# Optimization experiments

Hardware: AMD Instinct MI355X
Metric: run time of the kernel (lower is better)

The kernel has to match this reference:

```python
import jax, jax.numpy as jnp
import numpy as np
from jax import lax

TAU = 2.0      # LIF membrane time constant
VTH = 0.5      # spike threshold
ALPHA = 4.0    # sigmoid surrogate gradient sharpness (spikingjelly default)
EPS = 1e-5     # BatchNorm eps
HEADS = 8

@jax.custom_vjp
def _spike(x):
    return (x >= 0.0).astype(x.dtype)

def _spike_fwd(x):
    return _spike(x), x

def _spike_bwd(x, g):
    s = jax.nn.sigmoid(ALPHA * x)
    return (g * ALPHA * s * (1.0 - s),)

_spike.defvjp(_spike_fwd, _spike_bwd)

def lif(x_seq):
    # multi-step LIF, decay_input=True, hard reset to 0, detach_reset=True
    def step(v, x):
        v = v + (x - v) / TAU
        s = _spike(v - VTH)
        v = v * (1.0 - lax.stop_gradient(s))
        return v, s
    _, s_seq = lax.scan(step, jnp.zeros_like(x_seq[0]), x_seq)
    return s_seq

def bn(x, gamma, beta, mean, var):
    # inference-mode BatchNorm over channel axis 2 of [T,B,C,H,W]
    sh = (1, 1, -1, 1, 1)
    scale = gamma.reshape(sh) / jnp.sqrt(var.reshape(sh) + EPS)
    return (x - mean.reshape(sh)) * scale + beta.reshape(sh)

def conv1x1(x, w, b=None):
    y = jnp.einsum('oc,tbchw->tbohw', w, x)
    if b is not None:
        y = y + b.reshape(1, 1, -1, 1, 1)
    return y

def setup_inputs() -> dict:
    key = jax.random.key(0)
    T, B, C, H, W = 4, 8, 384, 32, 32
    ks = jax.random.split(key, 20)
    s = 1.0 / np.sqrt(C)
    d = {
        'x': jax.random.normal(ks[0], (T, B, C, H, W), jnp.float32),
        'q_w': jax.random.normal(ks[1], (C, C), jnp.float32) * s,
        'k_w': jax.random.normal(ks[2], (C, C), jnp.float32) * s,
        'v_w': jax.random.normal(ks[3], (C, C), jnp.float32) * s,
        'th_w': jax.random.normal(ks[4], (HEADS, HEADS), jnp.float32) * (1.0 / np.sqrt(HEADS)),
        'proj_w': jax.random.normal(ks[5], (C, C), jnp.float32) * s,
        'proj_b': jax.random.normal(ks[6], (C,), jnp.float32) * 0.01,
    }
    for i, p in enumerate(['q', 'k', 'v', 'proj']):
        kk = jax.random.split(ks[7 + i], 4)
        d[f'{p}_gamma'] = 1.0 + 0.1 * jax.random.normal(kk[0], (C,), jnp.float32)
        d[f'{p}_beta'] = 0.1 * jax.random.normal(kk[1], (C,), jnp.float32)
        d[f'{p}_mean'] = 0.1 * jax.random.normal(kk[2], (C,), jnp.float32)
        d[f'{p}_var'] = jax.random.uniform(kk[3], (C,), jnp.float32, 0.5, 1.5)
    return d

def reference(x, q_w, k_w, v_w, th_w, proj_w, proj_b,
              q_gamma, q_beta, q_mean, q_var,
              k_gamma, k_beta, k_mean, k_var,
              v_gamma, v_beta, v_mean, v_var,
              proj_gamma, proj_beta, proj_mean, proj_var):
    T, B, C, H, W = x.shape
    hd = C // HEADS
    N = H * W
    identity = x
    xs = lif(x)  # shortcut_lif

    def branch(w, g, be, m, va):
        return lif(bn(conv1x1(xs, w), g, be, m, va))

    def split_heads(t):  # [T,B,C,H,W] -> [T,B,heads,N,hd]
        return t.reshape(T, B, HEADS, hd, N).transpose(0, 1, 2, 4, 3)

    q = split_heads(branch(q_w, q_gamma, q_beta, q_mean, q_var))
    k = split_heads(branch(k_w, k_gamma, k_beta, k_mean, k_var))
    v = split_heads(branch(v_w, v_gamma, v_beta, v_mean, v_var))

    kv = (k * v).sum(axis=3)                      # [T,B,heads,hd]
    kv = jnp.einsum('oh,tbhd->tbod', th_w, kv)     # talking heads (Conv1d 1x1, no bias)
    kv = lif(kv)[:, :, :, None, :]                 # [T,B,heads,1,hd]

    x_att = q * kv                                 # broadcast over N
    x_att = x_att.transpose(0, 1, 2, 4, 3).reshape(T, B, C, H, W)
    out = bn(conv1x1(x_att, proj_w, proj_b), proj_gamma, proj_beta, proj_mean, proj_var)
    return out + identity
```

## Files before the change

### kernel.cpp

```cpp
#include <hip/hip_runtime.h>
#include <stdint.h>


typedef unsigned short u16;
typedef __attribute__((ext_vector_type(8))) short short8v;
typedef __attribute__((ext_vector_type(4))) float f32x4;

#define AS1 __attribute__((address_space(1)))
#define AS3 __attribute__((address_space(3)))

__device__ __forceinline__ void async16(const void* g, void* l) {
    __builtin_amdgcn_global_load_lds((const AS1 unsigned int*)g,
                                     (AS3 unsigned int*)l, 16, 0, 0);
}
__device__ __forceinline__ f32x4 mfma_bf16(short8v a, short8v b, f32x4 c) {
    return __builtin_amdgcn_mfma_f32_16x16x32_bf16(a, b, c, 0, 0, 0);
}
__device__ __forceinline__ f32x4 mfma_f16(short8v a, short8v b, f32x4 c) {
    return __builtin_amdgcn_mfma_f32_16x16x32_f16(a, b, c, 0, 0, 0);
}

__device__ __forceinline__ u16 f2bf(float f) {
    uint32_t x = __float_as_uint(f);
    return (u16)((x + 0x7FFFu + ((x >> 16) & 1u)) >> 16);
}

#define SPIKE_H ((u16)0x3C00)
#define SPIKE_B ((u16)0x3F80)

__global__ void prep_kernel(const float* __restrict__ qw, const float* __restrict__ kw,
                            const float* __restrict__ vw, const float* __restrict__ pw,
                            u16* __restrict__ Ah, u16* __restrict__ Aproj) {
    int id = blockIdx.x * 256 + threadIdx.x;
    if (id >= 1152 * 384) return;
    int m = id / 384, c = id % 384;
    int br = m / 384, o = m % 384;
    const float* W = (br == 0) ? qw : (br == 1) ? kw : vw;
    float w = W[o * 384 + c];
    union H { _Float16 h; u16 u; } u0, u1;
    u0.h = (_Float16)w;
    float r1 = w - (float)u0.h;
    u1.h = (_Float16)r1;
    u16* row = Ah + (size_t)m * 768;
    row[c] = u0.u;
    row[384 + c] = u1.u;
    if (br == 0) Aproj[o * 384 + c] = f2bf(pw[o * 384 + c]);
}

__global__ __launch_bounds__(256) void lifx_kernel(const float* __restrict__ x,
                                                   u16* __restrict__ xs) {
    __shared__ u16 Tr[64 * 72];
    int b = blockIdx.z, c0 = blockIdx.y * 64, n0 = blockIdx.x * 64;
    int tid = threadIdx.x;
    int nj = (tid & 15) * 4;
    int ci = tid >> 4;
    float v[4][4];
#pragma unroll
    for (int p = 0; p < 4; p++)
#pragma unroll
        for (int e = 0; e < 4; e++) v[p][e] = 0.0f;

    for (int t = 0; t < 4; t++) {
#pragma unroll
        for (int p = 0; p < 4; p++) {
            const float* src = x + ((size_t)((t * 8 + b) * 384 + c0 + p * 16 + ci)) * 1024 + n0 + nj;
            float4 xv = *(const float4*)src;
            float xa[4] = {xv.x, xv.y, xv.z, xv.w};
#pragma unroll
            for (int e = 0; e < 4; e++) {
                float vv = v[p][e];
                vv = __fadd_rn(vv, __fmul_rn(__fsub_rn(xa[e], vv), 0.5f));
                bool sp = (vv >= 0.5f);
                v[p][e] = sp ? 0.0f : vv;
                Tr[(nj + e) * 72 + p * 16 + ci] = sp ? SPIKE_H : (u16)0;
            }
        }
        __syncthreads();
#pragma unroll
        for (int p = 0; p < 4; p++) {
            int nr = p * 16 + (tid >> 4);
            int c4 = (tid & 15) * 4;
            *(ushort4*)(xs + ((size_t)((t * 8 + b) * 1024 + n0 + nr)) * 384 + c0 + c4) =
                *(const ushort4*)&Tr[nr * 72 + c4];
        }
        __syncthreads();
    }
}

__global__ __launch_bounds__(256, 2) void qkv_kernel(
    const u16* __restrict__ Ah, const u16* __restrict__ xs,
    u16* __restrict__ qs, u16* __restrict__ ks, u16* __restrict__ vs,
    const float* __restrict__ qg, const float* __restrict__ qb, const float* __restrict__ qm, const float* __restrict__ qv,
    const float* __restrict__ kg, const float* __restrict__ kb, const float* __restrict__ km, const float* __restrict__ kvr,
    const float* __restrict__ vg, const float* __restrict__ vb, const float* __restrict__ vm, const float* __restrict__ vvr) {
    __shared__ __align__(16) u16 At[2][8192];
    __shared__ __align__(16) u16 Bt[2][8192];
    __shared__ __align__(16) float bnS[128];
    __shared__ __align__(16) float bnM[128];
    __shared__ __align__(16) float bnB[128];

    int b = blockIdx.z, mt = blockIdx.y, nt = blockIdx.x;
    int m0 = mt * 128, n0 = nt * 128;
    int branch = mt / 3, o0 = (mt % 3) * 128;
    int tid = threadIdx.x, wave = tid >> 6, lane = tid & 63;
    int l15 = lane & 15, quad = lane >> 4;
    int wm = (wave & 1) * 64, wn = (wave >> 1) * 64;

    const float* g_ = (branch == 0) ? qg : (branch == 1) ? kg : vg;
    const float* be_ = (branch == 0) ? qb : (branch == 1) ? kb : vb;
    const float* m_ = (branch == 0) ? qm : (branch == 1) ? km : vm;
    const float* v_ = (branch == 0) ? qv : (branch == 1) ? kvr : vvr;
    u16* dstp = (branch == 0) ? qs : (branch == 1) ? ks : vs;

    if (tid < 128) {
        int o = o0 + tid;
        bnS[tid] = g_[o] / sqrtf(v_[o] + 1e-5f);
        bnM[tid] = m_[o];
        bnB[tid] = be_[o];
    }

    auto stage = [&](int s) {
        int st = s / 12, kkb = s % 12;
        int buf = s & 1;
        int kk = kkb * 64;
        int ck = (kk >= 384) ? kk - 384 : kk;
        const u16* Bsrc = xs + ((size_t)((st * 8 + b) * 1024 + n0)) * 384;
#pragma unroll
        for (int ii = 0; ii < 4; ii++) {
            int l = ii * 256 + tid;
            int row = l >> 3;
            int cs = (l & 7) ^ (row & 7);
            async16(Ah + (size_t)(m0 + row) * 768 + kk + cs * 8, &At[buf][l * 8]);
            async16(Bsrc + (size_t)row * 384 + ck + cs * 8, &Bt[buf][l * 8]);
        }
    };

    float vmem[4][4][4];
#pragma unroll
    for (int i = 0; i < 4; i++)
#pragma unroll
        for (int j = 0; j < 4; j++)
#pragma unroll
            for (int e = 0; e < 4; e++) vmem[i][j][e] = 0.0f;

    stage(0);
    __syncthreads();

    for (int t = 0; t < 4; t++) {
        f32x4 acc[4][4];
#pragma unroll
        for (int i = 0; i < 4; i++)
#pragma unroll
            for (int j = 0; j < 4; j++) acc[i][j] = (f32x4){0.f, 0.f, 0.f, 0.f};

        for (int kkb = 0; kkb < 12; kkb++) {
            int s = t * 12 + kkb;
            int buf = s & 1;
            if (s + 1 < 48) stage(s + 1);
#pragma unroll
            for (int h = 0; h < 2; h++) {
                short8v af[4], bfr[4];
#pragma unroll
                for (int i = 0; i < 4; i++) {
                    int row = wm + i * 16 + l15;
                    int ch = (h * 4 + quad) ^ (row & 7);
                    af[i] = *(const short8v*)&At[buf][row * 64 + ch * 8];
                }
#pragma unroll
                for (int j = 0; j < 4; j++) {
                    int nr = wn + j * 16 + l15;
                    int ch = (h * 4 + quad) ^ (nr & 7);
                    bfr[j] = *(const short8v*)&Bt[buf][nr * 64 + ch * 8];
                }
#pragma unroll
                for (int i = 0; i < 4; i++)
#pragma unroll
                    for (int j = 0; j < 4; j++) acc[i][j] = mfma_f16(af[i], bfr[j], acc[i][j]);
            }
            __syncthreads();
        }

        size_t rb = (size_t)((t * 8 + b) * 1024 + n0);
#pragma unroll
        for (int i = 0; i < 4; i++) {
            int co = wm + i * 16 + quad * 4;
            float4 sc4 = *(const float4*)&bnS[co];
            float4 mn4 = *(const float4*)&bnM[co];
            float4 bt4 = *(const float4*)&bnB[co];
            float scA[4] = {sc4.x, sc4.y, sc4.z, sc4.w};
            float mnA[4] = {mn4.x, mn4.y, mn4.z, mn4.w};
            float btA[4] = {bt4.x, bt4.y, bt4.z, bt4.w};
#pragma unroll
            for (int j = 0; j < 4; j++) {
                int n = wn + j * 16 + l15;
                u16 sv[4];
#pragma unroll
                for (int e = 0; e < 4; e++) {
                    float a = acc[i][j][e];
                    a = __fadd_rn(__fmul_rn(__fsub_rn(a, mnA[e]), scA[e]), btA[e]);
                    float vv = vmem[i][j][e];
                    vv = __fadd_rn(vv, __fmul_rn(__fsub_rn(a, vv), 0.5f));
                    bool sp = (vv >= 0.5f);
                    vmem[i][j][e] = sp ? 0.0f : vv;
                    sv[e] = sp ? SPIKE_B : (u16)0;
                }
                ushort4 s4;
                s4.x = sv[0]; s4.y = sv[1]; s4.z = sv[2]; s4.w = sv[3];
                *(ushort4*)(dstp + (rb + n) * 384 + o0 + co) = s4;
            }
        }
    }
}

__global__ void kvred_kernel(const u16* __restrict__ ks, const u16* __restrict__ vs,
                             float* __restrict__ r) {
    __shared__ float red[384];
    int tb = blockIdx.y, nc = blockIdx.x;
    int tid = threadIdx.x;
    int rr = tid / 48, c8 = tid % 48;
    red[tid] = 0.0f;
    __syncthreads();

    float cnt[8];
#pragma unroll
    for (int e = 0; e < 8; e++) cnt[e] = 0.0f;

    size_t base = ((size_t)(tb * 1024 + nc * 64 + rr)) * 384 + c8 * 8;
#pragma unroll 2
    for (int it = 0; it < 8; it++) {
        size_t off = base + (size_t)it * 8 * 384;
        uint4 ka = *(const uint4*)(ks + off);
        uint4 va = *(const uint4*)(vs + off);
        uint32_t w0 = ka.x & va.x, w1 = ka.y & va.y, w2 = ka.z & va.z, w3 = ka.w & va.w;
        const uint32_t S = SPIKE_B;
        if ((w0 & 0xFFFFu) == S) cnt[0] += 1.0f;
        if ((w0 >> 16) == S)     cnt[1] += 1.0f;
        if ((w1 & 0xFFFFu) == S) cnt[2] += 1.0f;
        if ((w1 >> 16) == S)     cnt[3] += 1.0f;
        if ((w2 & 0xFFFFu) == S) cnt[4] += 1.0f;
        if ((w2 >> 16) == S)     cnt[5] += 1.0f;
        if ((w3 & 0xFFFFu) == S) cnt[6] += 1.0f;
        if ((w3 >> 16) == S)     cnt[7] += 1.0f;
    }
#pragma unroll
    for (int e = 0; e < 8; e++) atomicAdd(&red[c8 * 8 + e], cnt[e]);
    __syncthreads();
    atomicAdd(&r[tb * 384 + tid], red[tid]);
}

__global__ void talking_kernel(const float* __restrict__ r, const float* __restrict__ th,
                               u16* __restrict__ kvs) {
    int id = blockIdx.x * 256 + threadIdx.x;
    if (id >= 8 * 384) return;
    int b = id / 384, c = id % 384;
    int oh = c / 48, d = c % 48;
    float v = 0.0f;
    for (int t = 0; t < 4; t++) {
        const float* rr = r + (t * 8 + b) * 384 + d;
        float s = 0.0f;
#pragma unroll
        for (int h = 0; h < 8; h++) s = __fmaf_rn(th[oh * 8 + h], rr[h * 48], s);
        v = __fadd_rn(v, __fmul_rn(__fsub_rn(s, v), 0.5f));
        bool sp = (v >= 0.5f);
        v = sp ? 0.0f : v;
        kvs[(t * 8 + b) * 384 + c] = sp ? SPIKE_B : (u16)0;
    }
}

__global__ __launch_bounds__(256, 2) void proj_kernel(
    const u16* __restrict__ Aproj, const u16* __restrict__ qs, const u16* __restrict__ kvs,
    const float* __restrict__ xin,
    const float* __restrict__ pb, const float* __restrict__ pg, const float* __restrict__ pbe,
    const float* __restrict__ pm, const float* __restrict__ pv, float* __restrict__ out) {
    __shared__ __align__(16) u16 At[2][8192];
    __shared__ __align__(16) u16 Bt[2][8192];

    int tb = blockIdx.z, mt = blockIdx.y, nt = blockIdx.x;
    int m0 = mt * 128, n0 = nt * 128;
    int tid = threadIdx.x, wave = tid >> 6, lane = tid & 63;
    int l15 = lane & 15, quad = lane >> 4;
    int wm = (wave & 1) * 64, wn = (wave >> 1) * 64;

    const u16* Bsrc = qs + ((size_t)(tb * 1024 + n0)) * 384;
    const u16* mbase = kvs + tb * 384;

    auto stage = [&](int s) {
        int kk = s * 64;
        int buf = s & 1;
#pragma unroll
        for (int ii = 0; ii < 4; ii++) {
            int l = ii * 256 + tid;
            int row = l >> 3;
            int cs = (l & 7) ^ (row & 7);
            async16(Aproj + (size_t)(m0 + row) * 384 + kk + cs * 8, &At[buf][l * 8]);
            async16(Bsrc + (size_t)row * 384 + kk + cs * 8, &Bt[buf][l * 8]);
        }
    };

    f32x4 acc[4][4];
#pragma unroll
    for (int i = 0; i < 4; i++)
#pragma unroll
        for (int j = 0; j < 4; j++) acc[i][j] = (f32x4){0.f, 0.f, 0.f, 0.f};

    stage(0);
    __syncthreads();

    for (int kkb = 0; kkb < 6; kkb++) {
        int buf = kkb & 1;
        int kk = kkb * 64;
        if (kkb + 1 < 6) stage(kkb + 1);
#pragma unroll
        for (int h = 0; h < 2; h++) {
            int g = h * 4 + quad;
            short8v msk = *(const short8v*)(mbase + kk + g * 8);
            short8v af[4], bfr[4];
#pragma unroll
            for (int i = 0; i < 4; i++) {
                int row = wm + i * 16 + l15;
                int ch = g ^ (row & 7);
                af[i] = *(const short8v*)&At[buf][row * 64 + ch * 8];
            }
#pragma unroll
            for (int j = 0; j < 4; j++) {
                int nr = wn + j * 16 + l15;
                int ch = g ^ (nr & 7);
                bfr[j] = *(const short8v*)&Bt[buf][nr * 64 + ch * 8] & msk;
            }
#pragma unroll
            for (int i = 0; i < 4; i++)
#pragma unroll
                for (int j = 0; j < 4; j++) acc[i][j] = mfma_bf16(af[i], bfr[j], acc[i][j]);
        }
        __syncthreads();
    }

#pragma unroll
    for (int i = 0; i < 4; i++) {
#pragma unroll
        for (int e = 0; e < 4; e++) {
            int o = m0 + wm + i * 16 + quad * 4 + e;
            float scale = pg[o] / sqrtf(pv[o] + 1e-5f);
            float mean = pm[o], beta = pbe[o], bias = pb[o];
#pragma unroll
            for (int j = 0; j < 4; j++) {
                int n = n0 + wn + j * 16 + l15;
                size_t idx = ((size_t)tb * 384 + o) * 1024 + n;
                float y = __fadd_rn(acc[i][j][e], bias);
                y = __fadd_rn(__fmul_rn(__fsub_rn(y, mean), scale), beta);
                out[idx] = __fadd_rn(y, xin[idx]);
            }
        }
    }
}

extern "C" void kernel_launch(void* const* d_in, const int* in_sizes, int n_in,
                              void* d_out, int out_size, void* d_ws, size_t ws_size,
                              hipStream_t stream) {
    (void)in_sizes; (void)n_in; (void)out_size; (void)ws_size;
    const float* x  = (const float*)d_in[0];
    const float* qw = (const float*)d_in[1];
    const float* kw = (const float*)d_in[2];
    const float* vw = (const float*)d_in[3];
    const float* th = (const float*)d_in[4];
    const float* pw = (const float*)d_in[5];
    const float* pb = (const float*)d_in[6];
    const float* qg = (const float*)d_in[7],  *qbe = (const float*)d_in[8];
    const float* qm = (const float*)d_in[9],  *qv  = (const float*)d_in[10];
    const float* kg = (const float*)d_in[11], *kbe = (const float*)d_in[12];
    const float* km = (const float*)d_in[13], *kv_ = (const float*)d_in[14];
    const float* vg = (const float*)d_in[15], *vbe = (const float*)d_in[16];
    const float* vm = (const float*)d_in[17], *vv_ = (const float*)d_in[18];
    const float* pg = (const float*)d_in[19], *pbe = (const float*)d_in[20];
    const float* pm = (const float*)d_in[21], *pv  = (const float*)d_in[22];
    float* out = (float*)d_out;

    char* w = (char*)d_ws;
    const size_t SPIKES = (size_t)32 * 1024 * 384 * 2;
    u16* xs    = (u16*)(w);
    u16* qs    = (u16*)(w + SPIKES);
    u16* ks    = (u16*)(w + 2 * SPIKES);
    u16* vs    = (u16*)(w + 3 * SPIKES);
    u16* Ah    = (u16*)(w + 4 * SPIKES);
    u16* Aproj = (u16*)(w + 4 * SPIKES + 1769472);
    float* r   = (float*)(w + 4 * SPIKES + 1769472 + 294912);
    u16* kvs   = (u16*)(w + 4 * SPIKES + 1769472 + 294912 + 49152);

    hipMemsetAsync(r, 0, 32 * 384 * sizeof(float), stream);

    prep_kernel<<<1728, 256, 0, stream>>>(qw, kw, vw, pw, Ah, Aproj);
    lifx_kernel<<<dim3(16, 6, 8), 256, 0, stream>>>(x, xs);
    qkv_kernel<<<dim3(8, 9, 8), 256, 0, stream>>>(Ah, xs, qs, ks, vs,
                                                  qg, qbe, qm, qv,
                                                  kg, kbe, km, kv_,
                                                  vg, vbe, vm, vv_);
    kvred_kernel<<<dim3(16, 32), 384, 0, stream>>>(ks, vs, r);
    talking_kernel<<<12, 256, 0, stream>>>(r, th, kvs);
    proj_kernel<<<dim3(8, 3, 32), 256, 0, stream>>>(Aproj, qs, kvs, x, pb, pg, pbe, pm, pv, out);
}
```

Before: 294.5 us.

## Replace LDS-staged GEMM tiles with direct global-to-register fragment loads

```diff
diff --git a/kernel.cpp b/kernel.cpp
--- a/kernel.cpp
+++ b/kernel.cpp
@@ -6,13 +6,6 @@
 typedef __attribute__((ext_vector_type(8))) short short8v;
 typedef __attribute__((ext_vector_type(4))) float f32x4;
 
-#define AS1 __attribute__((address_space(1)))
-#define AS3 __attribute__((address_space(3)))
-
-__device__ __forceinline__ void async16(const void* g, void* l) {
-    __builtin_amdgcn_global_load_lds((const AS1 unsigned int*)g,
-                                     (AS3 unsigned int*)l, 16, 0, 0);
-}
 __device__ __forceinline__ f32x4 mfma_bf16(short8v a, short8v b, f32x4 c) {
     return __builtin_amdgcn_mfma_f32_16x16x32_bf16(a, b, c, 0, 0, 0);
 }
@@ -87,24 +80,18 @@
     }
 }
 
-__global__ __launch_bounds__(256, 2) void qkv_kernel(
+__global__ __launch_bounds__(256) void qkv_kernel(
     const u16* __restrict__ Ah, const u16* __restrict__ xs,
     u16* __restrict__ qs, u16* __restrict__ ks, u16* __restrict__ vs,
     const float* __restrict__ qg, const float* __restrict__ qb, const float* __restrict__ qm, const float* __restrict__ qv,
     const float* __restrict__ kg, const float* __restrict__ kb, const float* __restrict__ km, const float* __restrict__ kvr,
     const float* __restrict__ vg, const float* __restrict__ vb, const float* __restrict__ vm, const float* __restrict__ vvr) {
-    __shared__ __align__(16) u16 At[2][8192];
-    __shared__ __align__(16) u16 Bt[2][8192];
-    __shared__ __align__(16) float bnS[128];
-    __shared__ __align__(16) float bnM[128];
-    __shared__ __align__(16) float bnB[128];
-
-    int b = blockIdx.z, mt = blockIdx.y, nt = blockIdx.x;
-    int m0 = mt * 128, n0 = nt * 128;
-    int branch = mt / 3, o0 = (mt % 3) * 128;
+    int b = blockIdx.z, mt = blockIdx.y;
     int tid = threadIdx.x, wave = tid >> 6, lane = tid & 63;
     int l15 = lane & 15, quad = lane >> 4;
-    int wm = (wave & 1) * 64, wn = (wave >> 1) * 64;
+    int m0 = mt * 64;
+    int branch = mt / 6, o0 = (mt % 6) * 64;
+    int n0 = blockIdx.x * 256 + wave * 64;
 
     const float* g_ = (branch == 0) ? qg : (branch == 1) ? kg : vg;
     const float* be_ = (branch == 0) ? qb : (branch == 1) ? kb : vb;
@@ -112,28 +99,7 @@
     const float* v_ = (branch == 0) ? qv : (branch == 1) ? kvr : vvr;
     u16* dstp = (branch == 0) ? qs : (branch == 1) ? ks : vs;
 
-    if (tid < 128) {
-        int o = o0 + tid;
-        bnS[tid] = g_[o] / sqrtf(v_[o] + 1e-5f);
-        bnM[tid] = m_[o];
-        bnB[tid] = be_[o];
-    }
-
-    auto stage = [&](int s) {
-        int st = s / 12, kkb = s % 12;
-        int buf = s & 1;
-        int kk = kkb * 64;
-        int ck = (kk >= 384) ? kk - 384 : kk;
-        const u16* Bsrc = xs + ((size_t)((st * 8 + b) * 1024 + n0)) * 384;
-#pragma unroll
-        for (int ii = 0; ii < 4; ii++) {
-            int l = ii * 256 + tid;
-            int row = l >> 3;
-            int cs = (l & 7) ^ (row & 7);
-            async16(Ah + (size_t)(m0 + row) * 768 + kk + cs * 8, &At[buf][l * 8]);
-            async16(Bsrc + (size_t)row * 384 + ck + cs * 8, &Bt[buf][l * 8]);
-        }
-    };
+    const u16* Abase = Ah + (size_t)(m0 + l15) * 768 + quad * 8;
 
     float vmem[4][4][4];
 #pragma unroll
@@ -143,56 +109,64 @@
 #pragma unroll
             for (int e = 0; e < 4; e++) vmem[i][j][e] = 0.0f;
 
-    stage(0);
-    __syncthreads();
-
     for (int t = 0; t < 4; t++) {
+        const u16* Bbase = xs + ((size_t)((t * 8 + b) * 1024 + n0 + l15)) * 384 + quad * 8;
+
         f32x4 acc[4][4];
 #pragma unroll
         for (int i = 0; i < 4; i++)
 #pragma unroll
             for (int j = 0; j < 4; j++) acc[i][j] = (f32x4){0.f, 0.f, 0.f, 0.f};
 
-        for (int kkb = 0; kkb < 12; kkb++) {
-            int s = t * 12 + kkb;
-            int buf = s & 1;
-            if (s + 1 < 48) stage(s + 1);
-#pragma unroll
-            for (int h = 0; h < 2; h++) {
-                short8v af[4], bfr[4];
-#pragma unroll
-                for (int i = 0; i < 4; i++) {
-                    int row = wm + i * 16 + l15;
-                    int ch = (h * 4 + quad) ^ (row & 7);
-                    af[i] = *(const short8v*)&At[buf][row * 64 + ch * 8];
-                }
-#pragma unroll
-                for (int j = 0; j < 4; j++) {
-                    int nr = wn + j * 16 + l15;
-                    int ch = (h * 4 + quad) ^ (nr & 7);
-                    bfr[j] = *(const short8v*)&Bt[buf][nr * 64 + ch * 8];
-                }
-#pragma unroll
-                for (int i = 0; i < 4; i++)
-#pragma unroll
-                    for (int j = 0; j < 4; j++) acc[i][j] = mfma_f16(af[i], bfr[j], acc[i][j]);
-            }
-            __syncthreads();
-        }
+        short8v Af[3][4], Bf[3][4];
+
+#define LOADF(HS, SLOT)                                                               \
+        {                                                                             \
+            const int kA = (HS) * 32;                                                 \
+            const int cB = ((HS) % 12) * 32;                                          \
+            _Pragma("unroll")                                                         \
+            for (int i = 0; i < 4; i++)                                               \
+                Af[SLOT][i] = *(const short8v*)(Abase + (size_t)i * (16 * 768) + kA); \
+            _Pragma("unroll")                                                         \
+            for (int j = 0; j < 4; j++)                                               \
+                Bf[SLOT][j] = *(const short8v*)(Bbase + (size_t)j * (16 * 384) + cB); \
+        }
+
+        LOADF(0, 0)
+        LOADF(1, 1)
+        LOADF(2, 2)
+
+#pragma unroll
+        for (int hs = 0; hs < 24; hs++) {
+            const int slot = hs % 3;
+#pragma unroll
+            for (int i = 0; i < 4; i++)
+#pragma unroll
+                for (int j = 0; j < 4; j++)
+                    acc[i][j] = mfma_f16(Af[slot][i], Bf[slot][j], acc[i][j]);
+            if (hs < 21) LOADF(hs + 3, slot)
+        }
+#undef LOADF
 
         size_t rb = (size_t)((t * 8 + b) * 1024 + n0);
 #pragma unroll
         for (int i = 0; i < 4; i++) {
-            int co = wm + i * 16 + quad * 4;
-            float4 sc4 = *(const float4*)&bnS[co];
-            float4 mn4 = *(const float4*)&bnM[co];
-            float4 bt4 = *(const float4*)&bnB[co];
-            float scA[4] = {sc4.x, sc4.y, sc4.z, sc4.w};
-            float mnA[4] = {mn4.x, mn4.y, mn4.z, mn4.w};
-            float btA[4] = {bt4.x, bt4.y, bt4.z, bt4.w};
+            int co = i * 16 + quad * 4;
+            int o = o0 + co;
+            float4 g4 = *(const float4*)(g_ + o);
+            float4 v4 = *(const float4*)(v_ + o);
+            float4 m4 = *(const float4*)(m_ + o);
+            float4 b4 = *(const float4*)(be_ + o);
+            float scA[4], mnA[4], btA[4];
+            scA[0] = g4.x / sqrtf(v4.x + 1e-5f);
+            scA[1] = g4.y / sqrtf(v4.y + 1e-5f);
+            scA[2] = g4.z / sqrtf(v4.z + 1e-5f);
+            scA[3] = g4.w / sqrtf(v4.w + 1e-5f);
+            mnA[0] = m4.x; mnA[1] = m4.y; mnA[2] = m4.z; mnA[3] = m4.w;
+            btA[0] = b4.x; btA[1] = b4.y; btA[2] = b4.z; btA[3] = b4.w;
 #pragma unroll
             for (int j = 0; j < 4; j++) {
-                int n = wn + j * 16 + l15;
+                int n = j * 16 + l15;
                 u16 sv[4];
 #pragma unroll
                 for (int e = 0; e < 4; e++) {
@@ -206,7 +180,7 @@
                 }
                 ushort4 s4;
                 s4.x = sv[0]; s4.y = sv[1]; s4.z = sv[2]; s4.w = sv[3];
-                *(ushort4*)(dstp + (rb + n) * 384 + o0 + co) = s4;
+                *(ushort4*)(dstp + (rb + n) * 384 + o) = s4;
             }
         }
     }
@@ -267,35 +241,20 @@
     }
 }
 
-__global__ __launch_bounds__(256, 2) void proj_kernel(
+__global__ __launch_bounds__(256) void proj_kernel(
     const u16* __restrict__ Aproj, const u16* __restrict__ qs, const u16* __restrict__ kvs,
     const float* __restrict__ xin,
     const float* __restrict__ pb, const float* __restrict__ pg, const float* __restrict__ pbe,
     const float* __restrict__ pm, const float* __restrict__ pv, float* __restrict__ out) {
-    __shared__ __align__(16) u16 At[2][8192];
-    __shared__ __align__(16) u16 Bt[2][8192];
-
-    int tb = blockIdx.z, mt = blockIdx.y, nt = blockIdx.x;
-    int m0 = mt * 128, n0 = nt * 128;
+    int tb = blockIdx.z, mt = blockIdx.y;
     int tid = threadIdx.x, wave = tid >> 6, lane = tid & 63;
     int l15 = lane & 15, quad = lane >> 4;
-    int wm = (wave & 1) * 64, wn = (wave >> 1) * 64;
-
-    const u16* Bsrc = qs + ((size_t)(tb * 1024 + n0)) * 384;
-    const u16* mbase = kvs + tb * 384;
-
-    auto stage = [&](int s) {
-        int kk = s * 64;
-        int buf = s & 1;
-#pragma unroll
-        for (int ii = 0; ii < 4; ii++) {
-            int l = ii * 256 + tid;
-            int row = l >> 3;
-            int cs = (l & 7) ^ (row & 7);
-            async16(Aproj + (size_t)(m0 + row) * 384 + kk + cs * 8, &At[buf][l * 8]);
-            async16(Bsrc + (size_t)row * 384 + kk + cs * 8, &Bt[buf][l * 8]);
-        }
-    };
+    int m0 = mt * 64;
+    int n0 = blockIdx.x * 256 + wave * 64;
+
+    const u16* Abase = Aproj + (size_t)(m0 + l15) * 384 + quad * 8;
+    const u16* Bbase = qs + ((size_t)(tb * 1024 + n0 + l15)) * 384 + quad * 8;
+    const u16* mbase = kvs + tb * 384 + quad * 8;
 
     f32x4 acc[4][4];
 #pragma unroll
@@ -303,48 +262,49 @@
 #pragma unroll
         for (int j = 0; j < 4; j++) acc[i][j] = (f32x4){0.f, 0.f, 0.f, 0.f};
 
-    stage(0);
-    __syncthreads();
-
-    for (int kkb = 0; kkb < 6; kkb++) {
-        int buf = kkb & 1;
-        int kk = kkb * 64;
-        if (kkb + 1 < 6) stage(kkb + 1);
-#pragma unroll
-        for (int h = 0; h < 2; h++) {
-            int g = h * 4 + quad;
-            short8v msk = *(const short8v*)(mbase + kk + g * 8);
-            short8v af[4], bfr[4];
-#pragma unroll
-            for (int i = 0; i < 4; i++) {
-                int row = wm + i * 16 + l15;
-                int ch = g ^ (row & 7);
-                af[i] = *(const short8v*)&At[buf][row * 64 + ch * 8];
-            }
-#pragma unroll
-            for (int j = 0; j < 4; j++) {
-                int nr = wn + j * 16 + l15;
-                int ch = g ^ (nr & 7);
-                bfr[j] = *(const short8v*)&Bt[buf][nr * 64 + ch * 8] & msk;
-            }
+    short8v Af[3][4], Bf[3][4], Mf[3];
+
+#define LOADP(HS, SLOT)                                                               \
+    {                                                                                 \
+        const int cB = (HS) * 32;                                                     \
+        _Pragma("unroll")                                                             \
+        for (int i = 0; i < 4; i++)                                                   \
+            Af[SLOT][i] = *(const short8v*)(Abase + (size_t)i * (16 * 384) + cB);     \
+        _Pragma("unroll")                                                             \
+        for (int j = 0; j < 4; j++)                                                   \
+            Bf[SLOT][j] = *(const short8v*)(Bbase + (size_t)j * (16 * 384) + cB);     \
+        Mf[SLOT] = *(const short8v*)(mbase + cB);                                     \
+    }
+
+    LOADP(0, 0)
+    LOADP(1, 1)
+    LOADP(2, 2)
+
+#pragma unroll
+    for (int hs = 0; hs < 12; hs++) {
+        const int slot = hs % 3;
+        short8v msk = Mf[slot];
+#pragma unroll
+        for (int j = 0; j < 4; j++) {
+            short8v bg = Bf[slot][j] & msk;
 #pragma unroll
             for (int i = 0; i < 4; i++)
-#pragma unroll
-                for (int j = 0; j < 4; j++) acc[i][j] = mfma_bf16(af[i], bfr[j], acc[i][j]);
-        }
-        __syncthreads();
-    }
+                acc[i][j] = mfma_bf16(Af[slot][i], bg, acc[i][j]);
+        }
+        if (hs < 9) LOADP(hs + 3, slot)
+    }
+#undef LOADP
 
 #pragma unroll
     for (int i = 0; i < 4; i++) {
 #pragma unroll
         for (int e = 0; e < 4; e++) {
-            int o = m0 + wm + i * 16 + quad * 4 + e;
+            int o = m0 + i * 16 + quad * 4 + e;
             float scale = pg[o] / sqrtf(pv[o] + 1e-5f);
             float mean = pm[o], beta = pbe[o], bias = pb[o];
 #pragma unroll
             for (int j = 0; j < 4; j++) {
-                int n = n0 + wn + j * 16 + l15;
+                int n = n0 + j * 16 + l15;
                 size_t idx = ((size_t)tb * 384 + o) * 1024 + n;
                 float y = __fadd_rn(acc[i][j][e], bias);
                 y = __fadd_rn(__fmul_rn(__fsub_rn(y, mean), scale), beta);
@@ -390,11 +350,11 @@
 
     prep_kernel<<<1728, 256, 0, stream>>>(qw, kw, vw, pw, Ah, Aproj);
     lifx_kernel<<<dim3(16, 6, 8), 256, 0, stream>>>(x, xs);
-    qkv_kernel<<<dim3(8, 9, 8), 256, 0, stream>>>(Ah, xs, qs, ks, vs,
-                                                  qg, qbe, qm, qv,
-                                                  kg, kbe, km, kv_,
-                                                  vg, vbe, vm, vv_);
+    qkv_kernel<<<dim3(4, 18, 8), 256, 0, stream>>>(Ah, xs, qs, ks, vs,
+                                                   qg, qbe, qm, qv,
+                                                   kg, kbe, km, kv_,
+                                                   vg, vbe, vm, vv_);
     kvred_kernel<<<dim3(16, 32), 384, 0, stream>>>(ks, vs, r);
     talking_kernel<<<12, 256, 0, stream>>>(r, th, kvs);
-    proj_kernel<<<dim3(8, 3, 32), 256, 0, stream>>>(Aproj, qs, kvs, x, pb, pg, pbe, pm, pv, out);
-}
+    proj_kernel<<<dim3(4, 6, 32), 256, 0, stream>>>(Aproj, qs, kvs, x, pb, pg, pbe, pm, pv, out);
+}
```

Result: slower. 512.1 us (+73.9%).
